# Optimization experiments

Measured on AMD Instinct MI355X. Metric: run time of the kernel, lower is better.

## Reference

```python
import jax, jax.numpy as jnp
import numpy as np

RCR = 5.2
RCA = 3.5
ETA_R = 16.0
SHF_R = jnp.asarray(np.linspace(0.9, 4.93125, 16), dtype=jnp.float32)  # 16 radial shifts
SHF_Z = jnp.asarray(np.array([0.19634954, 0.58904862, 0.9817477, 1.3744468,
                              1.7671459, 2.1598449, 2.552544, 2.9452431]), dtype=jnp.float32)
ETA_A = 8.0
ZETA = 32.0
SHF_A = jnp.asarray(np.array([0.9, 1.55, 2.2, 2.85]), dtype=jnp.float32)
NUM_SPECIES = 4  # consts file defines 4 species; module forces all atoms to species 0


def _cutoff(d, rc):
    return jnp.where(d <= rc, 0.5 * jnp.cos(jnp.pi * d / rc) + 0.5, 0.0)


def _aev(coords):
    n = coords.shape[0]
    diff = coords[:, None, :] - coords[None, :, :]             # [i,j,3]
    eye = jnp.eye(n, dtype=bool)
    d2 = jnp.sum(diff * diff, axis=-1)
    d = jnp.sqrt(jnp.where(eye, 1.0, d2))                      # safe sqrt on the diagonal
    # ---- radial subAEV: 0.25 * exp(-EtaR*(d-ShfR)^2) * fc(d, Rcr), summed over neighbors j
    fc_r = jnp.where(eye, 0.0, _cutoff(d, RCR))
    rad = 0.25 * jnp.exp(-ETA_R * (d[:, :, None] - SHF_R) ** 2) * fc_r[:, :, None]
    radial = jnp.sum(rad, axis=1)                              # (n, 16)
    # ---- angular subAEV
    fc_a = jnp.where(eye, 0.0, _cutoff(d, RCA))
    unit = diff / d[:, :, None]
    cos_t = jnp.einsum('ijc,ikc->ijk', unit, unit)             # cos angle(j-i-k)
    theta = jnp.arccos(0.95 * cos_t)                           # torchani's 0.95 stabilizer
    f1 = ((1.0 + jnp.cos(theta[..., None] - SHF_Z)) * 0.5) ** ZETA            # (n,n,n,8)
    davg = 0.5 * (d[:, :, None] + d[:, None, :])               # (d_ij + d_ik)/2
    # zero out j==i, k==i (via fc_a) and j==k; ordered (j,k) sum == torchani's 2*sum over j<k
    pairmask = (fc_a[:, :, None] * fc_a[:, None, :]) * (~eye)[None, :, :]
    f2 = jnp.exp(-ETA_A * (davg[..., None] - SHF_A) ** 2) * pairmask[..., None]  # (n,n,n,4)
    ang = jnp.einsum('ijka,ijkz->iaz', f2, f1).reshape(n, -1)  # (n, 32), (ShfA, ShfZ) order
    # ---- embed into 4-species AEV layout (only species-0 blocks are nonzero)
    radial_full = jnp.concatenate(
        [radial, jnp.zeros((n, 16 * (NUM_SPECIES - 1)), radial.dtype)], axis=1)   # (n, 64)
    n_pairs = NUM_SPECIES * (NUM_SPECIES + 1) // 2
    angular_full = jnp.concatenate(
        [ang, jnp.zeros((n, 32 * (n_pairs - 1)), ang.dtype)], axis=1)             # (n, 320)
    return jnp.concatenate([radial_full, angular_full], axis=1)                    # (n, 384)


def setup_inputs() -> dict:
    key = jax.random.key(0)
    # ~200-atom cluster, coordinates in Angstrom-scale cloud so cutoffs are populated
    coordinates = jax.random.normal(key, (200, 3), dtype=jnp.float32) * 4.0
    return {"coordinates": coordinates}


def reference(coordinates):
    return _aev(coordinates)
```

## Files before the change

kernel.cpp:

```cpp
#include <hip/hip_runtime.h>
#include <math.h>

#define RCR 5.2f
#define RCA 3.5f
#define ETA_R 16.0f
#define ETA_A 8.0f
#define PI_F 3.14159265358979323846f
#define MAXN 256

__global__ __launch_bounds__(256) void aev_kernel(const float* __restrict__ coords,
                                                  float* __restrict__ out, int n) {
    const int i = blockIdx.x;
    const int tid = threadIdx.x;

    __shared__ float sx[MAXN], sy[MAXN], sz[MAXN];
    __shared__ float nd[MAXN], nfca[MAXN], nux[MAXN], nuy[MAXN], nuz[MAXN];
    __shared__ int nb_cnt;
    __shared__ float s_rad[16];
    __shared__ float s_ang[32];

    for (int j = tid; j < n; j += blockDim.x) {
        sx[j] = coords[3 * j + 0];
        sy[j] = coords[3 * j + 1];
        sz[j] = coords[3 * j + 2];
    }
    if (tid == 0) nb_cnt = 0;
    if (tid < 16) s_rad[tid] = 0.0f;
    if (tid < 32) s_ang[tid] = 0.0f;
    __syncthreads();

    const float xi = sx[i], yi = sy[i], zi = sz[i];

    float racc[16];
#pragma unroll
    for (int r = 0; r < 16; r++) racc[r] = 0.0f;

    for (int j = tid; j < n; j += blockDim.x) {
        if (j == i) continue;
        const float dx = xi - sx[j];
        const float dy = yi - sy[j];
        const float dz = zi - sz[j];
        const float d = sqrtf(dx * dx + dy * dy + dz * dz);
        if (d <= RCR) {
            const float fcr = 0.5f * cosf(PI_F * d / RCR) + 0.5f;
#pragma unroll
            for (int r = 0; r < 16; r++) {
                const float t = d - (0.9f + 0.26875f * (float)r);
                racc[r] += expf(-ETA_R * t * t) * fcr;
            }
        }
        if (d <= RCA) {
            const int slot = atomicAdd(&nb_cnt, 1);
            const float inv = 1.0f / d;
            nd[slot] = d;
            nfca[slot] = 0.5f * cosf(PI_F * d / RCA) + 0.5f;
            nux[slot] = dx * inv;
            nuy[slot] = dy * inv;
            nuz[slot] = dz * inv;
        }
    }

#pragma unroll
    for (int r = 0; r < 16; r++) {
        float v = racc[r];
        for (int off = 32; off > 0; off >>= 1) v += __shfl_down(v, off);
        if ((tid & 63) == 0) atomicAdd(&s_rad[r], v);
    }
    __syncthreads();

    const int m = nb_cnt;

    const float shfZ[8] = {0.19634954f, 0.58904862f, 0.9817477f, 1.3744468f,
                           1.7671459f, 2.1598449f, 2.552544f, 2.9452431f};
    float cZ[8], sZ[8];
#pragma unroll
    for (int z = 0; z < 8; z++) {
        cZ[z] = cosf(shfZ[z]);
        sZ[z] = sinf(shfZ[z]);
    }

    float aacc[32];
#pragma unroll
    for (int c = 0; c < 32; c++) aacc[c] = 0.0f;

    const int npairs = m * m;
    for (int p = tid; p < npairs; p += blockDim.x) {
        const int j = p / m;
        const int k = p - j * m;
        if (j == k) continue;
        const float ct = 0.95f * (nux[j] * nux[k] + nuy[j] * nuy[k] + nuz[j] * nuz[k]);
        const float st = sqrtf(fmaxf(0.0f, 1.0f - ct * ct));
        const float davg = 0.5f * (nd[j] + nd[k]);
        const float fcp = nfca[j] * nfca[k];

        float f2[4];
#pragma unroll
        for (int a = 0; a < 4; a++) {
            const float t = davg - (0.9f + 0.65f * (float)a);
            f2[a] = expf(-ETA_A * t * t) * fcp;
        }
#pragma unroll
        for (int z = 0; z < 8; z++) {
            const float x = (1.0f + ct * cZ[z] + st * sZ[z]) * 0.5f;
            float t = x * x;
            t = t * t;
            t = t * t;
            t = t * t;
            t = t * t;
#pragma unroll
            for (int a = 0; a < 4; a++) aacc[a * 8 + z] += f2[a] * t;
        }
    }

#pragma unroll
    for (int c = 0; c < 32; c++) {
        float v = aacc[c];
        for (int off = 32; off > 0; off >>= 1) v += __shfl_down(v, off);
        if ((tid & 63) == 0) atomicAdd(&s_ang[c], v);
    }
    __syncthreads();

    float* row = out + (size_t)i * 384;
    for (int c = tid; c < 384; c += blockDim.x) {
        float v = 0.0f;
        if (c < 16) v = 0.25f * s_rad[c];
        else if (c >= 64 && c < 96) v = s_ang[c - 64];
        row[c] = v;
    }
}

extern "C" void kernel_launch(void* const* d_in, const int* in_sizes, int n_in,
                              void* d_out, int out_size, void* d_ws, size_t ws_size,
                              hipStream_t stream) {
    const float* coords = (const float*)d_in[0];
    float* out = (float*)d_out;
    const int n = in_sizes[0] / 3;
    aev_kernel<<<n, 256, 0, stream>>>(coords, out, n);
}
```

Before: 67.35 us.

## Halve angular pairs via j<k symmetry, ballot neighbor compaction, DPP reductions

The angular loop now iterates only over unordered pairs j<k, recovering the pair index from a triangular-number inversion, and doubles the result at output time. The shared-memory atomic neighbor counter is replaced by wave ballot/popcount prefix compaction into a packed float4 array. Cross-lane reductions use DPP row operations instead of shuffles, and cosf/expf become fast intrinsics with constant cos/sin tables. Each thread now handles exactly one atom, so the kernel assumes n <= 256, and the fast intrinsics trade some accuracy for speed.

```diff
diff --git a/kernel.cpp b/kernel.cpp
--- a/kernel.cpp
+++ b/kernel.cpp
@@ -8,123 +8,133 @@
 #define PI_F 3.14159265358979323846f
 #define MAXN 256
 
+template <int CTRL, int ROW_MASK>
+__device__ __forceinline__ float dpp_add(float v) {
+    int s = __builtin_amdgcn_update_dpp(0, __float_as_int(v), CTRL, ROW_MASK, 0xf, true);
+    return v + __int_as_float(s);
+}
+__device__ __forceinline__ float wave64_sum(float v) {
+    v = dpp_add<0x111, 0xf>(v);
+    v = dpp_add<0x112, 0xf>(v);
+    v = dpp_add<0x114, 0xf>(v);
+    v = dpp_add<0x118, 0xf>(v);
+    v = dpp_add<0x142, 0xa>(v);
+    v = dpp_add<0x143, 0xc>(v);
+    return v;
+}
+
 __global__ __launch_bounds__(256) void aev_kernel(const float* __restrict__ coords,
                                                   float* __restrict__ out, int n) {
     const int i = blockIdx.x;
     const int tid = threadIdx.x;
+    const int lane = tid & 63;
+    const int wv = tid >> 6;
 
     __shared__ float sx[MAXN], sy[MAXN], sz[MAXN];
-    __shared__ float nd[MAXN], nfca[MAXN], nux[MAXN], nuy[MAXN], nuz[MAXN];
-    __shared__ int nb_cnt;
+    __shared__ float4 njd[MAXN];
+    __shared__ float nfc[MAXN];
+    __shared__ int s_wcnt[4];
     __shared__ float s_rad[16];
     __shared__ float s_ang[32];
 
-    for (int j = tid; j < n; j += blockDim.x) {
-        sx[j] = coords[3 * j + 0];
-        sy[j] = coords[3 * j + 1];
-        sz[j] = coords[3 * j + 2];
+    if (tid < n) {
+        sx[tid] = coords[3 * tid + 0];
+        sy[tid] = coords[3 * tid + 1];
+        sz[tid] = coords[3 * tid + 2];
     }
-    if (tid == 0) nb_cnt = 0;
     if (tid < 16) s_rad[tid] = 0.0f;
     if (tid < 32) s_ang[tid] = 0.0f;
     __syncthreads();
 
     const float xi = sx[i], yi = sy[i], zi = sz[i];
 
+    const int j = tid;
+    const bool valid = (j < n) && (j != i);
+    float dx = 0.f, dy = 0.f, dz = 0.f, d = 1.0e9f;
+    if (valid) {
+        dx = xi - sx[j]; dy = yi - sy[j]; dz = zi - sz[j];
+        d = sqrtf(dx * dx + dy * dy + dz * dz);
+    }
+    const float fcr = (d <= RCR) ? (0.5f * __cosf(d * (PI_F / RCR)) + 0.5f) : 0.0f;
     float racc[16];
 #pragma unroll
-    for (int r = 0; r < 16; r++) racc[r] = 0.0f;
+    for (int r = 0; r < 16; r++) {
+        const float t = d - (0.9f + 0.26875f * (float)r);
+        racc[r] = fcr * __expf(-ETA_R * t * t);
+    }
 
-    for (int j = tid; j < n; j += blockDim.x) {
-        if (j == i) continue;
-        const float dx = xi - sx[j];
-        const float dy = yi - sy[j];
-        const float dz = zi - sz[j];
-        const float d = sqrtf(dx * dx + dy * dy + dz * dz);
-        if (d <= RCR) {
-            const float fcr = 0.5f * cosf(PI_F * d / RCR) + 0.5f;
+    const bool pred = valid && (d <= RCA);
+    const unsigned long long bmask = __ballot(pred);
+    if (lane == 0) s_wcnt[wv] = __popcll(bmask);
+    __syncthreads();
+    int base = 0;
 #pragma unroll
-            for (int r = 0; r < 16; r++) {
-                const float t = d - (0.9f + 0.26875f * (float)r);
-                racc[r] += expf(-ETA_R * t * t) * fcr;
-            }
-        }
-        if (d <= RCA) {
-            const int slot = atomicAdd(&nb_cnt, 1);
-            const float inv = 1.0f / d;
-            nd[slot] = d;
-            nfca[slot] = 0.5f * cosf(PI_F * d / RCA) + 0.5f;
-            nux[slot] = dx * inv;
-            nuy[slot] = dy * inv;
-            nuz[slot] = dz * inv;
-        }
+    for (int w = 0; w < 4; w++) if (w < wv) base += s_wcnt[w];
+    const int m = s_wcnt[0] + s_wcnt[1] + s_wcnt[2] + s_wcnt[3];
+    if (pred) {
+        const int slot = base + __popcll(bmask & ((1ULL << lane) - 1ULL));
+        const float inv = 1.0f / d;
+        njd[slot] = make_float4(dx * inv, dy * inv, dz * inv, d);
+        nfc[slot] = 0.5f * __cosf(d * (PI_F / RCA)) + 0.5f;
     }
 
 #pragma unroll
     for (int r = 0; r < 16; r++) {
-        float v = racc[r];
-        for (int off = 32; off > 0; off >>= 1) v += __shfl_down(v, off);
-        if ((tid & 63) == 0) atomicAdd(&s_rad[r], v);
+        const float v = wave64_sum(racc[r]);
+        if (lane == 63) atomicAdd(&s_rad[r], v);
     }
     __syncthreads();
 
-    const int m = nb_cnt;
-
-    const float shfZ[8] = {0.19634954f, 0.58904862f, 0.9817477f, 1.3744468f,
-                           1.7671459f, 2.1598449f, 2.552544f, 2.9452431f};
-    float cZ[8], sZ[8];
-#pragma unroll
-    for (int z = 0; z < 8; z++) {
-        cZ[z] = cosf(shfZ[z]);
-        sZ[z] = sinf(shfZ[z]);
-    }
-
+    const float cZ[8] = { 0.98078528f,  0.83146961f,  0.55557023f,  0.19509032f,
+                         -0.19509032f, -0.55557023f, -0.83146961f, -0.98078528f};
+    const float sZ[8] = { 0.19509032f,  0.55557023f,  0.83146961f,  0.98078528f,
+                          0.98078528f,  0.83146961f,  0.55557023f,  0.19509032f};
     float aacc[32];
 #pragma unroll
     for (int c = 0; c < 32; c++) aacc[c] = 0.0f;
 
-    const int npairs = m * m;
-    for (int p = tid; p < npairs; p += blockDim.x) {
-        const int j = p / m;
-        const int k = p - j * m;
-        if (j == k) continue;
-        const float ct = 0.95f * (nux[j] * nux[k] + nuy[j] * nuy[k] + nuz[j] * nuz[k]);
+    const int T = m * (m - 1) / 2;
+    for (int p = tid; p < T; p += 256) {
+        int jj = (int)((1.0f + sqrtf(8.0f * (float)p + 1.0f)) * 0.5f);
+        while (jj * (jj - 1) / 2 > p) jj--;
+        while ((jj + 1) * jj / 2 <= p) jj++;
+        const int kk = p - jj * (jj - 1) / 2;
+
+        const float4 a = njd[jj];
+        const float4 b = njd[kk];
+        const float ct = 0.95f * (a.x * b.x + a.y * b.y + a.z * b.z);
         const float st = sqrtf(fmaxf(0.0f, 1.0f - ct * ct));
-        const float davg = 0.5f * (nd[j] + nd[k]);
-        const float fcp = nfca[j] * nfca[k];
+        const float davg = 0.5f * (a.w + b.w);
+        const float fcp = nfc[jj] * nfc[kk];
 
         float f2[4];
 #pragma unroll
-        for (int a = 0; a < 4; a++) {
-            const float t = davg - (0.9f + 0.65f * (float)a);
-            f2[a] = expf(-ETA_A * t * t) * fcp;
+        for (int aa = 0; aa < 4; aa++) {
+            const float t = davg - (0.9f + 0.65f * (float)aa);
+            f2[aa] = fcp * __expf(-ETA_A * t * t);
         }
 #pragma unroll
         for (int z = 0; z < 8; z++) {
-            const float x = (1.0f + ct * cZ[z] + st * sZ[z]) * 0.5f;
-            float t = x * x;
-            t = t * t;
-            t = t * t;
-            t = t * t;
-            t = t * t;
+            const float x = fmaf(ct, cZ[z], fmaf(st, sZ[z], 1.0f)) * 0.5f;
+            float t2 = x * x; t2 *= t2; t2 *= t2; t2 *= t2; t2 *= t2;
 #pragma unroll
-            for (int a = 0; a < 4; a++) aacc[a * 8 + z] += f2[a] * t;
+            for (int aa = 0; aa < 4; aa++)
+                aacc[aa * 8 + z] = fmaf(f2[aa], t2, aacc[aa * 8 + z]);
         }
     }
 
 #pragma unroll
     for (int c = 0; c < 32; c++) {
-        float v = aacc[c];
-        for (int off = 32; off > 0; off >>= 1) v += __shfl_down(v, off);
-        if ((tid & 63) == 0) atomicAdd(&s_ang[c], v);
+        const float v = wave64_sum(aacc[c]);
+        if (lane == 63) atomicAdd(&s_ang[c], v);
     }
     __syncthreads();
 
     float* row = out + (size_t)i * 384;
-    for (int c = tid; c < 384; c += blockDim.x) {
+    for (int c = tid; c < 384; c += 256) {
         float v = 0.0f;
         if (c < 16) v = 0.25f * s_rad[c];
-        else if (c >= 64 && c < 96) v = s_ang[c - 64];
+        else if (c >= 64 && c < 96) v = 2.0f * s_ang[c - 64];
         row[c] = v;
     }
 }
```

Result: faster. 58.44 us (-13.2%).
